# Kernel tuning notes

Hardware: AMD Instinct MI355X
Metric: run time of the kernel (lower is better)

## Reference

```python
import jax, jax.numpy as jnp
import numpy as np

B, T, IN, H, OUT = 512, 1024, 16, 128, 1


def _lstm_layer(x_tbd, W_ih, W_hh, b_ih, b_hh):
    """Single LSTM layer, PyTorch gate order (i, f, g, o).
    x_tbd: [T, B, D_in] -> returns [T, B, H]."""
    Tn, Bn = x_tbd.shape[0], x_tbd.shape[1]
    # Precompute input contribution for all timesteps: [T, B, 4H]
    gx = jnp.einsum('tbd,gd->tbg', x_tbd, W_ih) + b_ih + b_hh
    h0 = jnp.zeros((Bn, H), x_tbd.dtype)
    c0 = jnp.zeros((Bn, H), x_tbd.dtype)

    def step(carry, gx_t):
        h, c = carry
        gates = gx_t + h @ W_hh.T  # [B, 4H]
        i = jax.nn.sigmoid(gates[:, 0 * H:1 * H])
        f = jax.nn.sigmoid(gates[:, 1 * H:2 * H])
        g = jnp.tanh(gates[:, 2 * H:3 * H])
        o = jax.nn.sigmoid(gates[:, 3 * H:4 * H])
        c = f * c + i * g
        h = o * jnp.tanh(c)
        return (h, c), h

    _, hs = jax.lax.scan(step, (h0, c0), gx)
    return hs  # [T, B, H]


def setup_inputs() -> dict:
    key = jax.random.key(0)
    ks = jax.random.split(key, 12)
    s = 1.0 / np.sqrt(H)  # PyTorch LSTM init scale
    return {
        'x': jax.random.normal(ks[0], (B, T, IN), jnp.float32),
        'W_ih0': jax.random.uniform(ks[1], (4 * H, IN), jnp.float32, -s, s),
        'W_hh0': jax.random.uniform(ks[2], (4 * H, H), jnp.float32, -s, s),
        'b_ih0': jax.random.uniform(ks[3], (4 * H,), jnp.float32, -s, s),
        'b_hh0': jax.random.uniform(ks[4], (4 * H,), jnp.float32, -s, s),
        'W_ih1': jax.random.uniform(ks[5], (4 * H, H), jnp.float32, -s, s),
        'W_hh1': jax.random.uniform(ks[6], (4 * H, H), jnp.float32, -s, s),
        'b_ih1': jax.random.uniform(ks[7], (4 * H,), jnp.float32, -s, s),
        'b_hh1': jax.random.uniform(ks[8], (4 * H,), jnp.float32, -s, s),
        'W_fc': jax.random.uniform(ks[9], (OUT, H), jnp.float32, -s, s),
        'b_fc': jax.random.uniform(ks[10], (OUT,), jnp.float32, -s, s),
    }


def reference(x, W_ih0, W_hh0, b_ih0, b_hh0, W_ih1, W_hh1, b_ih1, b_hh1, W_fc, b_fc):
    x_tbd = jnp.transpose(x, (1, 0, 2))  # [T, B, IN]
    h1 = _lstm_layer(x_tbd, W_ih0, W_hh0, b_ih0, b_hh0)  # [T, B, H]
    h2 = _lstm_layer(h1, W_ih1, W_hh1, b_ih1, b_hh1)     # [T, B, H]
    out = jnp.transpose(h2, (1, 0, 2))  # [B, T, H]
    out = jax.nn.relu(out)
    out = out @ W_fc.T + b_fc  # [B, T, 1]
    out = jax.nn.relu(out)
    return out
```

## Files before the change

### kernel.cpp

```cpp
#include <hip/hip_runtime.h>

#define T_SEQ  1024
#define NBATCH 512
#define IN_DIM 16
#define HDIM   128
#define G4     (4 * HDIM)
#define TC     64
#define NCHUNK (T_SEQ / TC)
#define NWGH   128

typedef unsigned short ushort_t;
typedef __attribute__((ext_vector_type(8))) _Float16 f16x8;
typedef __attribute__((ext_vector_type(4))) float f32x4;

#define MFMA16(a, b, c) __builtin_amdgcn_mfma_f32_16x16x32_f16((a), (b), (c), 0, 0, 0)

__device__ __forceinline__ float sigf(float x) {
  return __builtin_amdgcn_rcpf(1.0f + __expf(-x));
}
__device__ __forceinline__ float tanhf_fast(float x) {
  return 1.0f - 2.0f * __builtin_amdgcn_rcpf(1.0f + __expf(2.0f * x));
}
__device__ __forceinline__ ushort_t f16_bits(float f) {
  const _Float16 h = (_Float16)f;
  return __builtin_bit_cast(unsigned short, h);
}
__device__ __forceinline__ void split_f16(float f, ushort_t* hi, ushort_t* lo) {
  const _Float16 h = (_Float16)f;
  *hi = __builtin_bit_cast(unsigned short, h);
  const _Float16 l = (_Float16)(f - (float)h);
  *lo = __builtin_bit_cast(unsigned short, l);
}
__device__ __forceinline__ void bar_lds() {
  asm volatile("s_waitcnt lgkmcnt(0)\n\ts_barrier" ::: "memory");
}

__global__ __launch_bounds__(256) void prep_weights(
    const float* __restrict__ Whh0, const float* __restrict__ Whh1,
    const float* __restrict__ Wih0, const float* __restrict__ Wih1,
    ushort_t* __restrict__ w0h, ushort_t* __restrict__ w0l,
    ushort_t* __restrict__ w1h, ushort_t* __restrict__ w1l,
    ushort_t* __restrict__ wxh, ushort_t* __restrict__ wxl,
    ushort_t* __restrict__ wi1h, ushort_t* __restrict__ wi1l)
{
  const int idx = blockIdx.x * 256 + threadIdx.x;
  if (idx < 512 * HDIM) {
    split_f16(Whh0[idx], &w0h[idx], &w0l[idx]);
    split_f16(Whh1[idx], &w1h[idx], &w1l[idx]);
    split_f16(Wih1[idx], &wi1h[idx], &wi1l[idx]);
  }
  if (idx < 512 * 32) {
    const int g = idx >> 5, k = idx & 31;
    const float f = (k < IN_DIM) ? Wih0[g * IN_DIM + k] : 0.0f;
    split_f16(f, &wxh[idx], &wxl[idx]);
  }
}

__global__ __launch_bounds__(512, 2) void lstm_pipe(
    const float* __restrict__ x,
    const ushort_t* __restrict__ w0h,
    const ushort_t* __restrict__ wxh, const ushort_t* __restrict__ wxl,
    const float* __restrict__ bih0, const float* __restrict__ bhh0,
    const ushort_t* __restrict__ wi1h, const ushort_t* __restrict__ wi1l,
    const ushort_t* __restrict__ w1h,
    const float* __restrict__ bih1, const float* __restrict__ bhh1,
    const float* __restrict__ Wfc, const float* __restrict__ bfc,
    float* __restrict__ out,
    float* __restrict__ h1s, float* __restrict__ c1s,
    float* __restrict__ h2s, float* __restrict__ c2s,
    ushort_t* __restrict__ h1buf,
    float* __restrict__ gx1buf,
    int ch)
{
  const int tid  = threadIdx.x;
  const int lane = tid & 63;
  const int wv   = tid >> 6;
  const int row  = lane & 15;
  const int kq   = lane >> 4;
  const int bq   = row >> 2;
  const int j    = wv * 16 + row;

  if (blockIdx.x < NWGH) {
    if (ch >= NCHUNK) return;
    const int w  = blockIdx.x;
    const int b0 = w * 4;

    __shared__ __align__(16) ushort_t hfA[4][144], hfB[4][144];
    __shared__ __align__(16) ushort_t xlds[4][TC][32];

    f16x8 Bh[4][4], Bxh[4], Bxl[4];
#pragma unroll
    for (int i = 0; i < 4; ++i) {
      const int g = i * 128 + j;
#pragma unroll
      for (int kt = 0; kt < 4; ++kt)
        Bh[i][kt] = *(const f16x8*)&w0h[g * HDIM + kt * 32 + kq * 8];
      Bxh[i] = *(const f16x8*)&wxh[g * 32 + kq * 8];
      Bxl[i] = *(const f16x8*)&wxl[g * 32 + kq * 8];
    }

    {
      const int r = tid >> 1, half = tid & 1;
      const int b = r >> 6, ts = r & (TC - 1);
      const float* src =
          &x[((size_t)(b0 + b) * T_SEQ + ch * TC + ts) * IN_DIM + half * 8];
      const float4 v0 = *(const float4*)&src[0];
      const float4 v1 = *(const float4*)&src[4];
      ushort_t* dst = &xlds[b][ts][half * 8];
      dst[0] = f16_bits(v0.x); dst[1] = f16_bits(v0.y);
      dst[2] = f16_bits(v0.z); dst[3] = f16_bits(v0.w);
      dst[4] = f16_bits(v1.x); dst[5] = f16_bits(v1.y);
      dst[6] = f16_bits(v1.z); dst[7] = f16_bits(v1.w);
      *(float4*)&xlds[b][ts][16 + half * 8] = (float4){0.f, 0.f, 0.f, 0.f};
    }

    float bz[4];
#pragma unroll
    for (int i = 0; i < 4; ++i) bz[i] = bih0[i * 128 + j] + bhh0[i * 128 + j];
    float hc = h1s[(size_t)(b0 + kq) * HDIM + j];
    float cc = c1s[(size_t)(b0 + kq) * HDIM + j];
    hfA[kq][j] = f16_bits(hc);
    __syncthreads();

    ushort_t* hbp = h1buf + ((size_t)(ch & 1) * NWGH + w) * (TC * 4 * HDIM) +
                    (size_t)kq * HDIM + j;

#define L0_STEP(HIN, HOUT, TT)                                              \
  {                                                                         \
    const f16x8 ax = *(const f16x8*)&xlds[bq][TT][kq * 8];                  \
    f32x4 aH[4], aX[4];                                                     \
    _Pragma("unroll") for (int i = 0; i < 4; ++i) {                         \
      aH[i] = (f32x4){0.f, 0.f, 0.f, 0.f};                                  \
      aX[i] = (f32x4){0.f, 0.f, 0.f, 0.f};                                  \
    }                                                                       \
    _Pragma("unroll") for (int kt = 0; kt < 4; ++kt) {                      \
      const f16x8 ah = *(const f16x8*)&HIN[bq][kt * 32 + kq * 8];           \
      _Pragma("unroll") for (int i = 0; i < 4; ++i)                         \
          aH[i] = MFMA16(ah, Bh[i][kt], aH[i]);                             \
    }                                                                       \
    _Pragma("unroll") for (int i = 0; i < 4; ++i)                           \
        aX[i] = MFMA16(ax, Bxh[i], aX[i]);                                  \
    _Pragma("unroll") for (int i = 0; i < 4; ++i)                           \
        aX[i] = MFMA16(ax, Bxl[i], aX[i]);                                  \
    const float ig = sigf(aH[0][0] + aX[0][0] + bz[0]);                     \
    const float fg = sigf(aH[1][0] + aX[1][0] + bz[1]);                     \
    const float gg = tanhf_fast(aH[2][0] + aX[2][0] + bz[2]);               \
    const float og = sigf(aH[3][0] + aX[3][0] + bz[3]);                     \
    cc = fg * cc + ig * gg;                                                 \
    hc = og * tanhf_fast(cc);                                               \
    const ushort_t hbits = f16_bits(hc);                                    \
    HOUT[kq][j] = hbits;                                                    \
    *hbp = hbits;                                                           \
    hbp += 4 * HDIM;                                                        \
    bar_lds();                                                              \
  }

    for (int tt = 0; tt < TC; tt += 2) {
      L0_STEP(hfA, hfB, tt);
      L0_STEP(hfB, hfA, tt + 1);
    }
#undef L0_STEP

    h1s[(size_t)(b0 + kq) * HDIM + j] = hc;
    c1s[(size_t)(b0 + kq) * HDIM + j] = cc;
  } else {
    if (ch == 0) return;
    const int w  = blockIdx.x - NWGH;
    const int b0 = w * 4;

    __shared__ __align__(16) ushort_t hf1A[4][144], hf1B[4][144];
    __shared__ __align__(16) ushort_t h2l[TC][4][136];
    __shared__ float wfl[HDIM];

    const ushort_t* hb =
        h1buf + ((size_t)((ch - 1) & 1) * NWGH + w) * (TC * 4 * HDIM);
    float* gx = gx1buf + (size_t)w * (TC * 4 * HDIM * 4);

    if (tid < HDIM) wfl[tid] = Wfc[tid];

    {
      f16x8 Gh[4][4], Gl[4][4];
      float bz1[4];
#pragma unroll
      for (int i = 0; i < 4; ++i) {
        const int g = i * 128 + j;
#pragma unroll
        for (int kt = 0; kt < 4; ++kt) {
          const int off = g * HDIM + kt * 32 + kq * 8;
          Gh[i][kt] = *(const f16x8*)&wi1h[off];
          Gl[i][kt] = *(const f16x8*)&wi1l[off];
        }
        bz1[i] = bih1[i * 128 + j] + bhh1[i * 128 + j];
      }
#pragma unroll 2
      for (int mt = 0; mt < TC * 4 / 16; ++mt) {
        f32x4 acc[4];
#pragma unroll
        for (int i = 0; i < 4; ++i) acc[i] = (f32x4){0.f, 0.f, 0.f, 0.f};
#pragma unroll
        for (int kt = 0; kt < 4; ++kt) {
          const f16x8 a =
              *(const f16x8*)&hb[(size_t)(mt * 16 + row) * HDIM + kt * 32 + kq * 8];
#pragma unroll
          for (int i = 0; i < 4; ++i) acc[i] = MFMA16(a, Gh[i][kt], acc[i]);
#pragma unroll
          for (int i = 0; i < 4; ++i) acc[i] = MFMA16(a, Gl[i][kt], acc[i]);
        }
#pragma unroll
        for (int r = 0; r < 4; ++r) {
          const int m = mt * 16 + kq * 4 + r;
          float4 o;
          o.x = acc[0][r] + bz1[0];
          o.y = acc[1][r] + bz1[1];
          o.z = acc[2][r] + bz1[2];
          o.w = acc[3][r] + bz1[3];
          *(float4*)&gx[((size_t)m * HDIM + j) * 4] = o;
        }
      }
    }

    float hc = h2s[(size_t)(b0 + kq) * HDIM + j];
    float cc = c2s[(size_t)(b0 + kq) * HDIM + j];
    hf1A[kq][j] = f16_bits(hc);
    __syncthreads();

    f16x8 Rh[4][4];
#pragma unroll
    for (int i = 0; i < 4; ++i) {
      const int g = i * 128 + j;
#pragma unroll
      for (int kt = 0; kt < 4; ++kt)
        Rh[i][kt] = *(const f16x8*)&w1h[g * HDIM + kt * 32 + kq * 8];
    }

    const float4* gxp = (const float4*)&gx[((size_t)kq * HDIM + j) * 4];
    float4 zcc = *gxp;
    gxp += 512;

#define L1_STEP(HIN, HOUT, TT)                                              \
  {                                                                         \
    const float4 zcu = zcc;                                                 \
    if ((TT) + 1 < TC) { zcc = *gxp; gxp += 512; }                          \
    f32x4 aH[4];                                                            \
    _Pragma("unroll") for (int i = 0; i < 4; ++i)                           \
        aH[i] = (f32x4){0.f, 0.f, 0.f, 0.f};                                \
    _Pragma("unroll") for (int kt = 0; kt < 4; ++kt) {                      \
      const f16x8 ah = *(const f16x8*)&HIN[bq][kt * 32 + kq * 8];           \
      _Pragma("unroll") for (int i = 0; i < 4; ++i)                         \
          aH[i] = MFMA16(ah, Rh[i][kt], aH[i]);                             \
    }                                                                       \
    const float ig = sigf(aH[0][0] + zcu.x);                                \
    const float fg = sigf(aH[1][0] + zcu.y);                                \
    const float gg = tanhf_fast(aH[2][0] + zcu.z);                          \
    const float og = sigf(aH[3][0] + zcu.w);                                \
    cc = fg * cc + ig * gg;                                                 \
    hc = og * tanhf_fast(cc);                                               \
    const ushort_t hbits = f16_bits(hc);                                    \
    HOUT[kq][j] = hbits;                                                    \
    h2l[TT][kq][j] = hbits;                                                 \
    bar_lds();                                                              \
  }

    for (int tt = 0; tt < TC; tt += 2) {
      L1_STEP(hf1A, hf1B, tt);
      L1_STEP(hf1B, hf1A, tt + 1);
    }
#undef L1_STEP

    h2s[(size_t)(b0 + kq) * HDIM + j] = hc;
    c2s[(size_t)(b0 + kq) * HDIM + j] = cc;

    if (tid < TC * 4) {
      const int tt = tid >> 2, b = tid & 3;
      const float bfcv = bfc[0];
      float s0 = 0.f, s1 = 0.f, s2 = 0.f, s3 = 0.f;
#pragma unroll
      for (int q = 0; q < HDIM / 8; ++q) {
        const f16x8 hv = *(const f16x8*)&h2l[tt][b][q * 8];
        const float* wq = &wfl[q * 8];
        s0 += fmaxf((float)hv[0], 0.f) * wq[0];
        s1 += fmaxf((float)hv[1], 0.f) * wq[1];
        s2 += fmaxf((float)hv[2], 0.f) * wq[2];
        s3 += fmaxf((float)hv[3], 0.f) * wq[3];
        s0 += fmaxf((float)hv[4], 0.f) * wq[4];
        s1 += fmaxf((float)hv[5], 0.f) * wq[5];
        s2 += fmaxf((float)hv[6], 0.f) * wq[6];
        s3 += fmaxf((float)hv[7], 0.f) * wq[7];
      }
      const float s = s0 + s1 + s2 + s3 + bfcv;
      out[(size_t)(b0 + b) * T_SEQ + (ch - 1) * TC + tt] = fmaxf(s, 0.0f);
    }
  }
}

extern "C" void kernel_launch(void* const* d_in, const int* in_sizes, int n_in,
                              void* d_out, int out_size, void* d_ws, size_t ws_size,
                              hipStream_t stream)
{
  const float* x    = (const float*)d_in[0];
  const float* Wih0 = (const float*)d_in[1];
  const float* Whh0 = (const float*)d_in[2];
  const float* bih0 = (const float*)d_in[3];
  const float* bhh0 = (const float*)d_in[4];
  const float* Wih1 = (const float*)d_in[5];
  const float* Whh1 = (const float*)d_in[6];
  const float* bih1 = (const float*)d_in[7];
  const float* bhh1 = (const float*)d_in[8];
  const float* Wfc  = (const float*)d_in[9];
  const float* bfc  = (const float*)d_in[10];
  float* out = (float*)d_out;

  const size_t stateN = (size_t)NBATCH * HDIM;
  float* h1s = (float*)d_ws;
  float* c1s = h1s + stateN;
  float* h2s = c1s + stateN;
  float* c2s = h2s + stateN;
  ushort_t* w0h  = (ushort_t*)(c2s + stateN);
  ushort_t* w0l  = w0h  + stateN;
  ushort_t* w1h  = w0l  + stateN;
  ushort_t* w1l  = w1h  + stateN;
  ushort_t* wi1h = w1l  + stateN;
  ushort_t* wi1l = wi1h + stateN;
  ushort_t* wxh  = wi1l + stateN;
  ushort_t* wxl  = wxh  + 512 * 32;
  ushort_t* h1buf = wxl + 512 * 32;
  float* gx1buf = (float*)(h1buf + (size_t)2 * NWGH * TC * 4 * HDIM);

  (void)hipMemsetAsync(d_ws, 0, 4 * stateN * sizeof(float), stream);
  hipLaunchKernelGGL(prep_weights, dim3(256), dim3(256), 0, stream,
                     Whh0, Whh1, Wih0, Wih1,
                     w0h, w0l, w1h, w1l, wxh, wxl, wi1h, wi1l);

  for (int ch = 0; ch <= NCHUNK; ++ch) {
    hipLaunchKernelGGL(lstm_pipe, dim3(2 * NWGH), dim3(512), 0, stream,
                       x, w0h, wxh, wxl, bih0, bhh0,
                       wi1h, wi1l, w1h, bih1, bhh1, Wfc, bfc,
                       out, h1s, c1s, h2s, c2s, h1buf, gx1buf, ch);
  }
}
```

Before: 991.1 us.

## Batch layer-0 input projection per 8 steps and drop low-half W_ih1 MFMAs

Layer 0 now computes the x·W_ih0 input projection (hi+lo split) for 8 timesteps at once, using full 16-row MFMA tiles. The results go into a shared-memory gate buffer with the bias already added, so each recurrent step only runs the 16 W_hh MFMAs plus one LDS read instead of 8 extra input MFMAs. Layer 1's precomputed input projection drops the low-part f16 correction of W_ih1, which halves those MFMAs at some accuracy cost. Shared memory is unioned into one pool across the two block roles so the new buffer fits.

```diff
diff --git a/kernel.cpp b/kernel.cpp
--- a/kernel.cpp
+++ b/kernel.cpp
@@ -56,12 +56,25 @@
   }
 }
 
+struct L0LDS {
+  __align__(16) ushort_t hfA[4][144];
+  __align__(16) ushort_t hfB[4][144];
+  __align__(16) ushort_t xlds[4][TC][32];
+  __align__(16) float gx0s[8 * 4 * 128 * 4];
+};
+struct L1LDS {
+  __align__(16) ushort_t hfA[4][144];
+  __align__(16) ushort_t hfB[4][144];
+  __align__(16) ushort_t h2l[TC][4][136];
+  __align__(16) float wfl[HDIM];
+};
+
 __global__ __launch_bounds__(512, 2) void lstm_pipe(
     const float* __restrict__ x,
     const ushort_t* __restrict__ w0h,
     const ushort_t* __restrict__ wxh, const ushort_t* __restrict__ wxl,
     const float* __restrict__ bih0, const float* __restrict__ bhh0,
-    const ushort_t* __restrict__ wi1h, const ushort_t* __restrict__ wi1l,
+    const ushort_t* __restrict__ wi1h,
     const ushort_t* __restrict__ w1h,
     const float* __restrict__ bih1, const float* __restrict__ bhh1,
     const float* __restrict__ Wfc, const float* __restrict__ bfc,
@@ -80,13 +93,15 @@
   const int bq   = row >> 2;
   const int j    = wv * 16 + row;
 
+  constexpr size_t POOL =
+      sizeof(L0LDS) > sizeof(L1LDS) ? sizeof(L0LDS) : sizeof(L1LDS);
+  __shared__ __align__(16) char pool[POOL];
+
   if (blockIdx.x < NWGH) {
     if (ch >= NCHUNK) return;
+    L0LDS& S = *(L0LDS*)pool;
     const int w  = blockIdx.x;
     const int b0 = w * 4;
-
-    __shared__ __align__(16) ushort_t hfA[4][144], hfB[4][144];
-    __shared__ __align__(16) ushort_t xlds[4][TC][32];
 
     f16x8 Bh[4][4], Bxh[4], Bxl[4];
 #pragma unroll
@@ -106,12 +121,12 @@
           &x[((size_t)(b0 + b) * T_SEQ + ch * TC + ts) * IN_DIM + half * 8];
       const float4 v0 = *(const float4*)&src[0];
       const float4 v1 = *(const float4*)&src[4];
-      ushort_t* dst = &xlds[b][ts][half * 8];
+      ushort_t* dst = &S.xlds[b][ts][half * 8];
       dst[0] = f16_bits(v0.x); dst[1] = f16_bits(v0.y);
       dst[2] = f16_bits(v0.z); dst[3] = f16_bits(v0.w);
       dst[4] = f16_bits(v1.x); dst[5] = f16_bits(v1.y);
       dst[6] = f16_bits(v1.z); dst[7] = f16_bits(v1.w);
-      *(float4*)&xlds[b][ts][16 + half * 8] = (float4){0.f, 0.f, 0.f, 0.f};
+      *(float4*)&S.xlds[b][ts][16 + half * 8] = (float4){0.f, 0.f, 0.f, 0.f};
     }
 
     float bz[4];
@@ -119,7 +134,7 @@
     for (int i = 0; i < 4; ++i) bz[i] = bih0[i * 128 + j] + bhh0[i * 128 + j];
     float hc = h1s[(size_t)(b0 + kq) * HDIM + j];
     float cc = c1s[(size_t)(b0 + kq) * HDIM + j];
-    hfA[kq][j] = f16_bits(hc);
+    S.hfA[kq][j] = f16_bits(hc);
     __syncthreads();
 
     ushort_t* hbp = h1buf + ((size_t)(ch & 1) * NWGH + w) * (TC * 4 * HDIM) +
@@ -127,37 +142,58 @@
 
 #define L0_STEP(HIN, HOUT, TT)                                              \
   {                                                                         \
-    const f16x8 ax = *(const f16x8*)&xlds[bq][TT][kq * 8];                  \
-    f32x4 aH[4], aX[4];                                                     \
-    _Pragma("unroll") for (int i = 0; i < 4; ++i) {                         \
-      aH[i] = (f32x4){0.f, 0.f, 0.f, 0.f};                                  \
-      aX[i] = (f32x4){0.f, 0.f, 0.f, 0.f};                                  \
-    }                                                                       \
+    const float4 zcu =                                                      \
+        *(const float4*)&S.gx0s[((((TT) & 7) * 4 + kq) * 128 + j) * 4];     \
+    f32x4 aH[4];                                                            \
+    _Pragma("unroll") for (int i = 0; i < 4; ++i)                           \
+        aH[i] = (f32x4){0.f, 0.f, 0.f, 0.f};                                \
     _Pragma("unroll") for (int kt = 0; kt < 4; ++kt) {                      \
-      const f16x8 ah = *(const f16x8*)&HIN[bq][kt * 32 + kq * 8];           \
+      const f16x8 ah = *(const f16x8*)&S.HIN[bq][kt * 32 + kq * 8];         \
       _Pragma("unroll") for (int i = 0; i < 4; ++i)                         \
           aH[i] = MFMA16(ah, Bh[i][kt], aH[i]);                             \
     }                                                                       \
-    _Pragma("unroll") for (int i = 0; i < 4; ++i)                           \
-        aX[i] = MFMA16(ax, Bxh[i], aX[i]);                                  \
-    _Pragma("unroll") for (int i = 0; i < 4; ++i)                           \
-        aX[i] = MFMA16(ax, Bxl[i], aX[i]);                                  \
-    const float ig = sigf(aH[0][0] + aX[0][0] + bz[0]);                     \
-    const float fg = sigf(aH[1][0] + aX[1][0] + bz[1]);                     \
-    const float gg = tanhf_fast(aH[2][0] + aX[2][0] + bz[2]);               \
-    const float og = sigf(aH[3][0] + aX[3][0] + bz[3]);                     \
+    const float ig = sigf(aH[0][0] + zcu.x);                                \
+    const float fg = sigf(aH[1][0] + zcu.y);                                \
+    const float gg = tanhf_fast(aH[2][0] + zcu.z);                          \
+    const float og = sigf(aH[3][0] + zcu.w);                                \
     cc = fg * cc + ig * gg;                                                 \
     hc = og * tanhf_fast(cc);                                               \
     const ushort_t hbits = f16_bits(hc);                                    \
-    HOUT[kq][j] = hbits;                                                    \
+    S.HOUT[kq][j] = hbits;                                                  \
     *hbp = hbits;                                                           \
     hbp += 4 * HDIM;                                                        \
     bar_lds();                                                              \
   }
 
-    for (int tt = 0; tt < TC; tt += 2) {
-      L0_STEP(hfA, hfB, tt);
-      L0_STEP(hfB, hfA, tt + 1);
+    for (int sc = 0; sc < TC / 8; ++sc) {
+#pragma unroll
+      for (int mt = 0; mt < 2; ++mt) {
+        const f16x8 a =
+            *(const f16x8*)&S.xlds[row & 3][sc * 8 + mt * 4 + (row >> 2)][kq * 8];
+        f32x4 acc[4];
+#pragma unroll
+        for (int i = 0; i < 4; ++i) acc[i] = (f32x4){0.f, 0.f, 0.f, 0.f};
+#pragma unroll
+        for (int i = 0; i < 4; ++i) acc[i] = MFMA16(a, Bxh[i], acc[i]);
+#pragma unroll
+        for (int i = 0; i < 4; ++i) acc[i] = MFMA16(a, Bxl[i], acc[i]);
+#pragma unroll
+        for (int r = 0; r < 4; ++r) {
+          float4 o;
+          o.x = acc[0][r] + bz[0];
+          o.y = acc[1][r] + bz[1];
+          o.z = acc[2][r] + bz[2];
+          o.w = acc[3][r] + bz[3];
+          *(float4*)&S.gx0s[(((mt * 4 + kq) * 4 + r) * 128 + j) * 4] = o;
+        }
+      }
+      bar_lds();
+#pragma unroll 1
+      for (int q = 0; q < 4; ++q) {
+        const int tt = sc * 8 + q * 2;
+        L0_STEP(hfA, hfB, tt);
+        L0_STEP(hfB, hfA, tt + 1);
+      }
     }
 #undef L0_STEP
 
@@ -165,31 +201,25 @@
     c1s[(size_t)(b0 + kq) * HDIM + j] = cc;
   } else {
     if (ch == 0) return;
+    L1LDS& S = *(L1LDS*)pool;
     const int w  = blockIdx.x - NWGH;
     const int b0 = w * 4;
-
-    __shared__ __align__(16) ushort_t hf1A[4][144], hf1B[4][144];
-    __shared__ __align__(16) ushort_t h2l[TC][4][136];
-    __shared__ float wfl[HDIM];
 
     const ushort_t* hb =
         h1buf + ((size_t)((ch - 1) & 1) * NWGH + w) * (TC * 4 * HDIM);
     float* gx = gx1buf + (size_t)w * (TC * 4 * HDIM * 4);
 
-    if (tid < HDIM) wfl[tid] = Wfc[tid];
+    if (tid < HDIM) S.wfl[tid] = Wfc[tid];
 
     {
-      f16x8 Gh[4][4], Gl[4][4];
+      f16x8 Gh[4][4];
       float bz1[4];
 #pragma unroll
       for (int i = 0; i < 4; ++i) {
         const int g = i * 128 + j;
 #pragma unroll
-        for (int kt = 0; kt < 4; ++kt) {
-          const int off = g * HDIM + kt * 32 + kq * 8;
-          Gh[i][kt] = *(const f16x8*)&wi1h[off];
-          Gl[i][kt] = *(const f16x8*)&wi1l[off];
-        }
+        for (int kt = 0; kt < 4; ++kt)
+          Gh[i][kt] = *(const f16x8*)&wi1h[g * HDIM + kt * 32 + kq * 8];
         bz1[i] = bih1[i * 128 + j] + bhh1[i * 128 + j];
       }
 #pragma unroll 2
@@ -203,8 +233,6 @@
               *(const f16x8*)&hb[(size_t)(mt * 16 + row) * HDIM + kt * 32 + kq * 8];
 #pragma unroll
           for (int i = 0; i < 4; ++i) acc[i] = MFMA16(a, Gh[i][kt], acc[i]);
-#pragma unroll
-          for (int i = 0; i < 4; ++i) acc[i] = MFMA16(a, Gl[i][kt], acc[i]);
         }
 #pragma unroll
         for (int r = 0; r < 4; ++r) {
@@ -221,7 +249,7 @@
 
     float hc = h2s[(size_t)(b0 + kq) * HDIM + j];
     float cc = c2s[(size_t)(b0 + kq) * HDIM + j];
-    hf1A[kq][j] = f16_bits(hc);
+    S.hfA[kq][j] = f16_bits(hc);
     __syncthreads();
 
     f16x8 Rh[4][4];
@@ -245,7 +273,7 @@
     _Pragma("unroll") for (int i = 0; i < 4; ++i)                           \
         aH[i] = (f32x4){0.f, 0.f, 0.f, 0.f};                                \
     _Pragma("unroll") for (int kt = 0; kt < 4; ++kt) {                      \
-      const f16x8 ah = *(const f16x8*)&HIN[bq][kt * 32 + kq * 8];           \
+      const f16x8 ah = *(const f16x8*)&S.HIN[bq][kt * 32 + kq * 8];         \
       _Pragma("unroll") for (int i = 0; i < 4; ++i)                         \
           aH[i] = MFMA16(ah, Rh[i][kt], aH[i]);                             \
     }                                                                       \
@@ -256,14 +284,14 @@
     cc = fg * cc + ig * gg;                                                 \
     hc = og * tanhf_fast(cc);                                               \
     const ushort_t hbits = f16_bits(hc);                                    \
-    HOUT[kq][j] = hbits;                                                    \
-    h2l[TT][kq][j] = hbits;                                                 \
+    S.HOUT[kq][j] = hbits;                                                  \
+    S.h2l[TT][kq][j] = hbits;                                               \
     bar_lds();                                                              \
   }
 
     for (int tt = 0; tt < TC; tt += 2) {
-      L1_STEP(hf1A, hf1B, tt);
-      L1_STEP(hf1B, hf1A, tt + 1);
+      L1_STEP(hfA, hfB, tt);
+      L1_STEP(hfB, hfA, tt + 1);
     }
 #undef L1_STEP
 
@@ -276,8 +304,8 @@
       float s0 = 0.f, s1 = 0.f, s2 = 0.f, s3 = 0.f;
 #pragma unroll
       for (int q = 0; q < HDIM / 8; ++q) {
-        const f16x8 hv = *(const f16x8*)&h2l[tt][b][q * 8];
-        const float* wq = &wfl[q * 8];
+        const f16x8 hv = *(const f16x8*)&S.h2l[tt][b][q * 8];
+        const float* wq = &S.wfl[q * 8];
         s0 += fmaxf((float)hv[0], 0.f) * wq[0];
         s1 += fmaxf((float)hv[1], 0.f) * wq[1];
         s2 += fmaxf((float)hv[2], 0.f) * wq[2];
@@ -334,7 +362,7 @@
   for (int ch = 0; ch <= NCHUNK; ++ch) {
     hipLaunchKernelGGL(lstm_pipe, dim3(2 * NWGH), dim3(512), 0, stream,
                        x, w0h, wxh, wxl, bih0, bhh0,
-                       wi1h, wi1l, w1h, bih1, bhh1, Wfc, bfc,
+                       wi1h, w1h, bih1, bhh1, Wfc, bfc,
                        out, h1s, c1s, h2s, c2s, h1buf, gx1buf, ch);
   }
 }
```

Result: faster. 926.7 us (-6.5%).
